# Kernel optimization log

Measured on AMD Instinct MI355X. Metric: run time of the kernel, lower is better.

The kernel has to match this reference:

```python
import jax, jax.numpy as jnp
from jax import lax
import numpy as np

DN = ('NCHW', 'OIHW', 'NCHW')

def conv(x, w, b, stride, pad):
    y = lax.conv_general_dilated(x, w, (stride, stride), [(pad, pad), (pad, pad)], dimension_numbers=DN)
    return y + b[None, :, None, None]

def conv_t(x, w, b, stride, pad):
    # PyTorch ConvTranspose2d weight layout is (in, out, kh, kw); flip spatially, swap to OIHW,
    # and realize transpose-conv as lhs-dilated conv with padding k-1-p.
    k = w.shape[2]
    wt = jnp.flip(w, (2, 3)).transpose(1, 0, 2, 3)
    q = k - 1 - pad
    y = lax.conv_general_dilated(x, wt, (1, 1), [(q, q), (q, q)], lhs_dilation=(stride, stride), dimension_numbers=DN)
    return y + b[None, :, None, None]

def setup_inputs() -> dict:
    key = jax.random.key(0)
    ks = jax.random.split(key, 16)
    K, C = 512, 64
    def he(k, shape, fan_in):
        return jax.random.normal(k, shape, jnp.float32) * np.float32(np.sqrt(2.0 / fan_in))
    return {
        'x': jax.random.normal(ks[0], (64, 1, 256, 256), jnp.float32),
        'e1_w': he(ks[1], (32, 1, 4, 4), 1 * 16), 'e1_b': jnp.zeros((32,), jnp.float32),
        'e2_w': he(ks[2], (64, 32, 4, 4), 32 * 16), 'e2_b': jnp.zeros((64,), jnp.float32),
        'e3_w': he(ks[3], (64, 64, 3, 3), 64 * 9), 'e3_b': jnp.zeros((64,), jnp.float32),
        'emb': jax.random.uniform(ks[4], (K, C), jnp.float32, -1.0 / K, 1.0 / K),
        'd1_w': he(ks[5], (64, 32, 3, 3), 64 * 9), 'd1_b': jnp.zeros((32,), jnp.float32),
        'd2_w': he(ks[6], (32, 64, 4, 4), 32 * 16), 'd2_b': jnp.zeros((64,), jnp.float32),
        'd3_w': he(ks[7], (64, 1, 4, 4), 64 * 16), 'd3_b': jnp.zeros((1,), jnp.float32),
    }

def reference(x, e1_w, e1_b, e2_w, e2_b, e3_w, e3_b, emb, d1_w, d1_b, d2_w, d2_b, d3_w, d3_b):
    # encoder
    h = jax.nn.relu(conv(x, e1_w, e1_b, 2, 1))
    h = jax.nn.relu(conv(h, e2_w, e2_b, 2, 1))
    ze = jax.nn.relu(conv(h, e3_w, e3_b, 1, 1))  # (N, C, H, W)
    N, C, H, W = ze.shape
    # VQ: nearest codebook entry per spatial location via ||z||^2 - 2 z.e + ||e||^2
    zf = ze.transpose(0, 2, 3, 1).reshape(-1, C)  # (N*H*W, C)
    dist = (zf * zf).sum(-1, keepdims=True) - 2.0 * (zf @ emb.T) + (emb * emb).sum(-1)[None, :]
    idx = jnp.argmin(dist, axis=1)  # (N*H*W,)
    zq = emb[idx].reshape(N, H, W, C).transpose(0, 3, 1, 2)  # (N, C, H, W)
    # straight-through estimator
    dec_in = ze + lax.stop_gradient(zq - ze)
    # decoder
    h = jax.nn.relu(conv_t(dec_in, d1_w, d1_b, 1, 1))
    h = jax.nn.relu(conv_t(h, d2_w, d2_b, 2, 1))
    x_hat = conv_t(h, d3_w, d3_b, 2, 1)
    return (x_hat, ze, zq)
```

## Files before the change

kernel.cpp:

```cpp
#include <hip/hip_runtime.h>

typedef short short8 __attribute__((ext_vector_type(8)));
typedef float f32x4 __attribute__((ext_vector_type(4)));

union U8 { short8 s8; unsigned int u[4]; };

__device__ __forceinline__ unsigned short f2bf(float f) {
    unsigned int u = __float_as_uint(f);
    u = (u + 0x7fffu + ((u >> 16) & 1u)) >> 16;
    return (unsigned short)u;
}
__device__ __forceinline__ float bf2f(unsigned short s) {
    return __uint_as_float(((unsigned int)s) << 16);
}


__global__ __launch_bounds__(256) void k_e1i(
    const float* __restrict__ x, const float* __restrict__ e1w, const float* __restrict__ e1b,
    unsigned short* __restrict__ h1p2, unsigned int* __restrict__ ws_dw,
    const float* __restrict__ e2w, const float* __restrict__ e3w,
    const float* __restrict__ d1w, const float* __restrict__ d2w,
    const float* __restrict__ d3w, const float* __restrict__ emb,
    unsigned short* __restrict__ ape2, unsigned short* __restrict__ ape3,
    unsigned short* __restrict__ apd1, unsigned short* __restrict__ apd2,
    unsigned short* __restrict__ apd3, unsigned short* __restrict__ embbf,
    float* __restrict__ hninit)
{
    int bid = blockIdx.x;
    if (bid < 4096) {
        int idx = bid * 256 + threadIdx.x;
        int ow = idx & 127, oh = (idx >> 7) & 127, n = idx >> 14;
        const float* xn = x + (size_t)n * 65536;
        float patch[16];
#pragma unroll
        for (int kh = 0; kh < 4; kh++) {
            int ih = 2 * oh + kh - 1;
#pragma unroll
            for (int kw = 0; kw < 4; kw++) {
                int iw = 2 * ow + kw - 1;
                bool ok = ((unsigned)ih < 256u) & ((unsigned)iw < 256u);
                patch[kh * 4 + kw] = ok ? xn[ih * 256 + iw] : 0.f;
            }
        }
        unsigned int outw[16];
#pragma unroll
        for (int oc = 0; oc < 32; oc++) {
            float acc = e1b[oc];
#pragma unroll
            for (int t = 0; t < 16; t++) acc += patch[t] * e1w[oc * 16 + t];
            unsigned short bf = f2bf(fmaxf(acc, 0.f));
            if (oc & 1) outw[oc >> 1] |= ((unsigned int)bf) << 16;
            else        outw[oc >> 1] = bf;
        }
        int par = ow & 1;
        int cidx = (ow + par) >> 1;
        size_t base = ((size_t)((idx >> 14) * 130 + oh + 1) * 2 + par) * 2112 + cidx * 32;
        uint4* dst = (uint4*)(h1p2 + base);
#pragma unroll
        for (int i = 0; i < 4; i++) dst[i] = *(uint4*)&outw[i * 4];
        return;
    }
    if (bid < 11376) {
        int t = (bid - 4096) * 256 + threadIdx.x;
        if (t < 270336) {
            int img = t / 4224, q = t % 4224;
            int rowsel = q / 2112, rem = q % 2112;
            ws_dw[img * 274560 + rowsel * 129 * 2112 + rem] = 0u;
        } else if (t < 532480) {
            int g = t - 270336;
            int img = g / 4096, q = g % 4096;
            int row = 1 + (q >> 5), c2 = q & 31;
            int sel = c2 >> 4, ch = c2 & 15;
            int par = sel ? 0 : 1, idx2 = sel ? 64 : 0;
            ws_dw[img * 274560 + row * 2112 + par * 1056 + idx2 * 16 + ch] = 0u;
        } else if (t < 1863680) {
            unsigned int base, Cd, r;
            if (t < 1064960)      { base = 17571840u; Cd = 32; r = t - 532480;  }
            else if (t < 1597440) { base = 34881536u; Cd = 32; r = t - 1064960; }
            else                  { base = 43802624u; Cd = 16; r = t - 1597440; }
            unsigned int per_img = 260u * Cd;
            unsigned int img = r / per_img, q = r % per_img;
            unsigned int p = q / Cd, c = q % Cd;
            unsigned int row, col;
            if (p < 66u)        { row = 0;  col = p; }
            else if (p < 132u)  { row = 65; col = p - 66u; }
            else { unsigned int s = p - 132u; row = 1 + (s >> 1); col = (s & 1) ? 65u : 0u; }
            ws_dw[base + ((img * 66u + row) * 66u + col) * Cd + c] = 0u;
        }
        return;
    }
    int f = (bid - 11376) * 256 + threadIdx.x;
    if (f < 4096) {
        int ks = f >> 8, mt = (f >> 6) & 3, lane = f & 63;
        int quad = lane >> 4, l16 = lane & 15;
        int oc = mt * 16 + l16, kh = ks >> 2, kw = ks & 3;
        short8 sv;
#pragma unroll
        for (int j = 0; j < 8; j++) {
            int ic = quad * 8 + j;
            sv[j] = (short)f2bf(e2w[((oc * 32 + ic) * 4 + kh) * 4 + kw]);
        }
        ((short8*)ape2)[f] = sv;
    } else if (f < 8704) {
        int g = f - 4096;
        int ks = g >> 8, mt = (g >> 6) & 3, lane = g & 63;
        int quad = lane >> 4, l16 = lane & 15;
        int oc = mt * 16 + l16, tap = ks >> 1, kh = tap / 3, kw = tap % 3;
        int icb = (ks & 1) * 32 + quad * 8;
        short8 sv;
#pragma unroll
        for (int j = 0; j < 8; j++)
            sv[j] = (short)f2bf(e3w[((oc * 64 + icb + j) * 3 + kh) * 3 + kw]);
        ((short8*)ape3)[g] = sv;
    } else if (f < 11008) {
        int g = f - 8704;
        int ks = g >> 7, mt = (g >> 6) & 1, lane = g & 63;
        int quad = lane >> 4, l16 = lane & 15;
        int oc = mt * 16 + l16, tap = ks >> 1, kh = tap / 3, kw = tap % 3;
        int icb = (ks & 1) * 32 + quad * 8;
        short8 sv;
#pragma unroll
        for (int j = 0; j < 8; j++)
            sv[j] = (short)f2bf(d1w[(((icb + j) * 32 + oc) * 3 + (2 - kh)) * 3 + (2 - kw)]);
        ((short8*)apd1)[g] = sv;
    } else if (f < 15104) {
        int g = f - 11008;
        int par = g >> 10, ks = (g >> 8) & 3, mt = (g >> 6) & 3, lane = g & 63;
        int quad = lane >> 4, l16 = lane & 15;
        int ph = par >> 1, pw = par & 1, a = ks >> 1, bb = ks & 1;
        int kh = 3 - ph - 2 * a, kw = 3 - pw - 2 * bb;
        int oc = mt * 16 + l16;
        short8 sv;
#pragma unroll
        for (int j = 0; j < 8; j++) {
            int ic = quad * 8 + j;
            sv[j] = (short)f2bf(d2w[((ic * 64 + oc) * 4 + kh) * 4 + kw]);
        }
        ((short8*)apd2)[g] = sv;
    } else if (f < 15232) {
        int g = f - 15104;
        int ks = g >> 6, lane = g & 63;
        int quad = lane >> 4, tap = lane & 15;
        short8 sv;
#pragma unroll
        for (int j = 0; j < 8; j++) {
            int ic = ks * 32 + quad * 8 + j;
            sv[j] = (short)f2bf(d3w[ic * 16 + tap]);
        }
        ((short8*)apd3)[g] = sv;
    } else if (f < 19328) {
        int g = f - 15232;
        int code = g >> 3, chb = (g & 7) * 8;
        short8 sv;
#pragma unroll
        for (int j = 0; j < 8; j++) sv[j] = (short)f2bf(emb[code * 64 + chb + j]);
        ((short8*)embbf)[g] = sv;
    } else if (f < 19840) {
        int code = f - 19328;
        float s = 0.f;
        for (int c = 0; c < 64; c++) { float v = emb[code * 64 + c]; s += v * v; }
        hninit[code] = 2.0f - 0.5f * s;
    }
}

template<int CIN, int COUT, int KSTEPS, int NCH, int WPIN, int MODE>
__global__ __launch_bounds__(256, 4) void k_conv(const unsigned short* __restrict__ inp,
                                                 const unsigned short* __restrict__ aprep,
                                                 const float* __restrict__ bias,
                                                 unsigned short* __restrict__ out0) {
    constexpr int MT = COUT / 16;
    constexpr int KCH = KSTEPS / NCH;
    __shared__ short8 sA[KCH * MT * 64];
    int tid = threadIdx.x;
    int wave = tid >> 6, lane = tid & 63, quad = lane >> 4, l16 = lane & 15;
    int bid = blockIdx.x;
    int n = bid >> 4, rg = bid & 15;
    int oh = rg * 4 + wave;

    int base0;
    if (MODE == 0) base0 = (n * 130 + 2 * oh) * 4224 + quad * 8;
    else           base0 = n * (WPIN * WPIN * CIN) + ((oh + 1) * WPIN + 1) * CIN + quad * 8;

    f32x4 acc[4][MT];
#pragma unroll
    for (int t = 0; t < 4; t++)
#pragma unroll
        for (int mt = 0; mt < MT; mt++)
            acc[t][mt] = *(const f32x4*)(bias + mt * 16 + quad * 4);

#pragma unroll
    for (int ch = 0; ch < NCH; ch++) {
        for (int i = tid; i < KCH * MT * 64; i += 256)
            sA[i] = ((const short8*)aprep)[ch * (KCH * MT * 64) + i];
        __syncthreads();
#pragma unroll
        for (int k = 0; k < KCH; k++) {
            int ks = ch * KCH + k;
            int off, pxs;
            if (MODE == 0) {
                int kh = ks >> 2, kw = ks & 3;
                int par = (kw & 1) ^ 1;
                off = kh * 4224 + par * 2112 + (kw >> 1) * 32;
                pxs = 32;
            } else {
                int tap = ks >> 1, kh = tap / 3, kw = tap % 3;
                off = ((kh - 1) * WPIN + (kw - 1)) * CIN + (ks & 1) * 32;
                pxs = CIN;
            }
            short8 bfr[4];
#pragma unroll
            for (int t = 0; t < 4; t++)
                bfr[t] = *(const short8*)(inp + base0 + (t * 16 + l16) * pxs + off);
#pragma unroll
            for (int mt = 0; mt < MT; mt++) {
                short8 a = sA[(k * MT + mt) * 64 + lane];
#pragma unroll
                for (int t = 0; t < 4; t++)
                    acc[t][mt] = __builtin_amdgcn_mfma_f32_16x16x32_bf16(a, bfr[t], acc[t][mt], 0, 0, 0);
            }
        }
        if (ch + 1 < NCH) __syncthreads();
    }

#pragma unroll
    for (int t = 0; t < 4; t++) {
        int ow = t * 16 + l16;
#pragma unroll
        for (int mt = 0; mt < MT; mt++) {
            float v0 = fmaxf(acc[t][mt][0], 0.f), v1 = fmaxf(acc[t][mt][1], 0.f);
            float v2 = fmaxf(acc[t][mt][2], 0.f), v3 = fmaxf(acc[t][mt][3], 0.f);
            unsigned int lo = (unsigned int)f2bf(v0) | ((unsigned int)f2bf(v1) << 16);
            unsigned int hi = (unsigned int)f2bf(v2) | ((unsigned int)f2bf(v3) << 16);
            uint2 uu; uu.x = lo; uu.y = hi;
            int oc = mt * 16 + quad * 4;
            if (MODE == 0) {
                size_t addr = (size_t)n * 278784 + ((oh + 1) * 66 + ow + 1) * 64 + oc;
                *(uint2*)(out0 + addr) = uu;
            } else {
                size_t addr = (size_t)n * 139392 + ((oh + 1) * 66 + ow + 1) * 32 + oc;
                *(uint2*)(out0 + addr) = uu;
            }
        }
    }
}

__global__ __launch_bounds__(256, 4) void k_e3vq(const unsigned short* __restrict__ h2p,
                                                 const unsigned short* __restrict__ ape3,
                                                 const float* __restrict__ bias,
                                                 const unsigned short* __restrict__ embbf,
                                                 const float* __restrict__ hninit,
                                                 float* __restrict__ ze_out,
                                                 float* __restrict__ zq_out,
                                                 unsigned short* __restrict__ zqp) {
    __shared__ __align__(16) char smem[36864];
    short8* sA = (short8*)smem;
    char*   sC = smem;

    int tid = threadIdx.x;
    int wave = tid >> 6, lane = tid & 63, quad = lane >> 4, l16 = lane & 15;
    int bid = blockIdx.x;
    int n = bid >> 4, rg = bid & 15;
    int oh = rg * 4 + wave;
    int base0 = n * 278784 + ((oh + 1) * 66 + 1) * 64 + quad * 8;

    f32x4 acc[4][4];
#pragma unroll
    for (int t = 0; t < 4; t++)
#pragma unroll
        for (int mt = 0; mt < 4; mt++)
            acc[t][mt] = *(const f32x4*)(bias + mt * 16 + quad * 4);

#pragma unroll
    for (int ch = 0; ch < 2; ch++) {
        for (int i = tid; i < 9 * 4 * 64; i += 256)
            sA[i] = ((const short8*)ape3)[ch * (9 * 4 * 64) + i];
        __syncthreads();
#pragma unroll
        for (int k = 0; k < 9; k++) {
            int ks = ch * 9 + k;
            int tap = ks >> 1, kh = tap / 3, kw = tap % 3;
            int off = ((kh - 1) * 66 + (kw - 1)) * 64 + (ks & 1) * 32;
            short8 bfr[4];
#pragma unroll
            for (int t = 0; t < 4; t++)
                bfr[t] = *(const short8*)(h2p + base0 + (t * 16 + l16) * 64 + off);
#pragma unroll
            for (int mt = 0; mt < 4; mt++) {
                short8 a = sA[(k * 4 + mt) * 64 + lane];
#pragma unroll
                for (int t = 0; t < 4; t++)
                    acc[t][mt] = __builtin_amdgcn_mfma_f32_16x16x32_bf16(a, bfr[t], acc[t][mt], 0, 0, 0);
            }
        }
        if (ch == 0) __syncthreads();
    }

#pragma unroll
    for (int t = 0; t < 4; t++)
#pragma unroll
        for (int mt = 0; mt < 4; mt++)
#pragma unroll
            for (int r = 0; r < 4; r++)
                acc[t][mt][r] = fmaxf(acc[t][mt][r], 0.f);

#pragma unroll
    for (int t = 0; t < 4; t++) {
        int px = oh * 64 + t * 16 + l16;
#pragma unroll
        for (int mt = 0; mt < 4; mt++) {
            int oc = mt * 16 + quad * 4;
#pragma unroll
            for (int r = 0; r < 4; r++)
                __builtin_nontemporal_store(acc[t][mt][r], &ze_out[((size_t)n * 64 + oc + r) * 4096 + px]);
        }
    }

    short8 b0[4], b1[4];
    int s0 = (((2 * quad) & 3) << 4) | l16;
    int s1 = (((2 * quad + 1) & 3) << 4) | l16;
#pragma unroll
    for (int t = 0; t < 4; t++) {
        f32x4 xv = (quad < 2) ? acc[t][0] : acc[t][1];
        f32x4 yv = (quad < 2) ? acc[t][2] : acc[t][3];
        unsigned int xa = (unsigned int)f2bf(xv[0]) | ((unsigned int)f2bf(xv[1]) << 16);
        unsigned int xb = (unsigned int)f2bf(xv[2]) | ((unsigned int)f2bf(xv[3]) << 16);
        unsigned int ya = (unsigned int)f2bf(yv[0]) | ((unsigned int)f2bf(yv[1]) << 16);
        unsigned int yb = (unsigned int)f2bf(yv[2]) | ((unsigned int)f2bf(yv[3]) << 16);
        U8 ub0, ub1;
        ub0.u[0] = (unsigned int)__shfl((int)xa, s0); ub0.u[1] = (unsigned int)__shfl((int)xb, s0);
        ub0.u[2] = (unsigned int)__shfl((int)xa, s1); ub0.u[3] = (unsigned int)__shfl((int)xb, s1);
        ub1.u[0] = (unsigned int)__shfl((int)ya, s0); ub1.u[1] = (unsigned int)__shfl((int)yb, s0);
        ub1.u[2] = (unsigned int)__shfl((int)ya, s1); ub1.u[3] = (unsigned int)__shfl((int)yb, s1);
        b0[t] = ub0.s8; b1[t] = ub1.s8;
    }

    unsigned int bk[4] = {0u, 0u, 0u, 0u};
#pragma unroll 1
    for (int cb = 0; cb < 4; cb++) {
        __syncthreads();
        {
            int r = tid >> 1, h = tid & 1;
            const uint4* src = (const uint4*)embbf;
#pragma unroll
            for (int i = 0; i < 4; i++) {
                uint4 v = src[cb * 1024 + tid * 4 + i];
                int slot = 4 * h + i;
                *(uint4*)(sC + r * 128 + ((slot ^ (r & 7)) << 4)) = v;
            }
        }
        __syncthreads();
#pragma unroll 2
        for (int jj = 0; jj < 8; jj++) {
            int j0 = cb * 128 + jj * 16;
            int rr = jj * 16 + l16;
            int sw = (rr & 7) << 4;
            short8 a0 = *(const short8*)(sC + rr * 128 + (((quad << 4)) ^ sw));
            short8 a1 = *(const short8*)(sC + rr * 128 + ((((quad + 4) << 4)) ^ sw));
            f32x4 ci = *(const f32x4*)(hninit + j0 + quad * 4);
            int iv = 511 - j0 - quad * 4;
#pragma unroll
            for (int t = 0; t < 4; t++) {
                f32x4 s = __builtin_amdgcn_mfma_f32_16x16x32_bf16(a0, b0[t], ci, 0, 0, 0);
                s = __builtin_amdgcn_mfma_f32_16x16x32_bf16(a1, b1[t], s, 0, 0, 0);
#pragma unroll
                for (int r = 0; r < 4; r++) {
                    unsigned int key = (__float_as_uint(s[r]) & 0xFFFFFE00u) | (unsigned int)(iv - r);
                    bk[t] = bk[t] > key ? bk[t] : key;
                }
            }
        }
    }
#pragma unroll
    for (int t = 0; t < 4; t++) {
        unsigned int o1 = (unsigned int)__shfl_xor((int)bk[t], 16);
        bk[t] = bk[t] > o1 ? bk[t] : o1;
        unsigned int o2 = (unsigned int)__shfl_xor((int)bk[t], 32);
        bk[t] = bk[t] > o2 ? bk[t] : o2;
    }
#pragma unroll
    for (int t = 0; t < 4; t++) {
        int code = 511 - (int)(bk[t] & 511u);
        int col = t * 16 + l16;
        int hw = oh * 64 + col;
        uint4 u0 = *(const uint4*)(embbf + code * 64 + quad * 16);
        uint4 u1 = *(const uint4*)(embbf + code * 64 + quad * 16 + 8);
        size_t qaddr = (size_t)n * 278784 + ((oh + 1) * 66 + (col + 1)) * 64 + quad * 16;
        *(uint4*)(zqp + qaddr) = u0;
        *(uint4*)(zqp + qaddr + 8) = u1;
        size_t zb = ((size_t)n * 64 + quad * 16) * 4096 + hw;
        unsigned int uw[8] = {u0.x, u0.y, u0.z, u0.w, u1.x, u1.y, u1.z, u1.w};
#pragma unroll
        for (int i = 0; i < 8; i++) {
            __builtin_nontemporal_store(__uint_as_float(uw[i] << 16), &zq_out[zb + (2 * i + 0) * 4096]);
            __builtin_nontemporal_store(__uint_as_float(uw[i] & 0xFFFF0000u), &zq_out[zb + (2 * i + 1) * 4096]);
        }
    }
}

__global__ __launch_bounds__(256, 4) void k_d2f(const unsigned short* __restrict__ d1op,
                                                const unsigned short* __restrict__ apd2,
                                                const float* __restrict__ bias,
                                                const unsigned short* __restrict__ apd3,
                                                unsigned short* __restrict__ sc16) {
    __shared__ short8 sA[1024];
    int tid = threadIdx.x;
    int wave = tid >> 6, lane = tid & 63, quad = lane >> 4, l16 = lane & 15;
    int bid = blockIdx.x;
    int n = bid >> 6, par = (bid >> 4) & 3, rg = bid & 15;
    int oh = rg * 4 + wave;
    int ph = par >> 1, pw = par & 1;

    short8 pa0 = ((const short8*)apd3)[lane];
    short8 pa1 = ((const short8*)apd3)[64 + lane];

    for (int i = tid; i < 1024; i += 256) sA[i] = ((const short8*)apd2)[par * 1024 + i];
    __syncthreads();

    int base0 = n * 139392 + ((oh + ph) * 66 + pw) * 32 + quad * 8;
    f32x4 acc[4][4];
#pragma unroll
    for (int t = 0; t < 4; t++)
#pragma unroll
        for (int mt = 0; mt < 4; mt++)
            acc[t][mt] = *(const f32x4*)(bias + mt * 16 + quad * 4);

#pragma unroll
    for (int k = 0; k < 4; k++) {
        int a_ = k >> 1, bb = k & 1;
        int off = (a_ * 66 + bb) * 32;
        short8 bfr[4];
#pragma unroll
        for (int t = 0; t < 4; t++)
            bfr[t] = *(const short8*)(d1op + base0 + (t * 16 + l16) * 32 + off);
#pragma unroll
        for (int mt = 0; mt < 4; mt++) {
            short8 a = sA[(k * 4 + mt) * 64 + lane];
#pragma unroll
            for (int t = 0; t < 4; t++)
                acc[t][mt] = __builtin_amdgcn_mfma_f32_16x16x32_bf16(a, bfr[t], acc[t][mt], 0, 0, 0);
        }
    }

    int s0 = (((2 * quad) & 3) << 4) | l16;
    int s1 = (((2 * quad + 1) & 3) << 4) | l16;
    int oh_out = 2 * oh + ph;
#pragma unroll
    for (int t = 0; t < 4; t++) {
#pragma unroll
        for (int mt = 0; mt < 4; mt++)
#pragma unroll
            for (int r = 0; r < 4; r++)
                acc[t][mt][r] = fmaxf(acc[t][mt][r], 0.f);
        f32x4 xv = (quad < 2) ? acc[t][0] : acc[t][1];
        f32x4 yv = (quad < 2) ? acc[t][2] : acc[t][3];
        unsigned int xa = (unsigned int)f2bf(xv[0]) | ((unsigned int)f2bf(xv[1]) << 16);
        unsigned int xb = (unsigned int)f2bf(xv[2]) | ((unsigned int)f2bf(xv[3]) << 16);
        unsigned int ya = (unsigned int)f2bf(yv[0]) | ((unsigned int)f2bf(yv[1]) << 16);
        unsigned int yb = (unsigned int)f2bf(yv[2]) | ((unsigned int)f2bf(yv[3]) << 16);
        U8 ub0, ub1;
        ub0.u[0] = (unsigned int)__shfl((int)xa, s0); ub0.u[1] = (unsigned int)__shfl((int)xb, s0);
        ub0.u[2] = (unsigned int)__shfl((int)xa, s1); ub0.u[3] = (unsigned int)__shfl((int)xb, s1);
        ub1.u[0] = (unsigned int)__shfl((int)ya, s0); ub1.u[1] = (unsigned int)__shfl((int)yb, s0);
        ub1.u[2] = (unsigned int)__shfl((int)ya, s1); ub1.u[3] = (unsigned int)__shfl((int)yb, s1);
        f32x4 sc = {0.f, 0.f, 0.f, 0.f};
        sc = __builtin_amdgcn_mfma_f32_16x16x32_bf16(pa0, ub0.s8, sc, 0, 0, 0);
        sc = __builtin_amdgcn_mfma_f32_16x16x32_bf16(pa1, ub1.s8, sc, 0, 0, 0);
        int ow_out = 2 * (t * 16 + l16) + pw;
        int pbaseo = n * 16384 + oh_out * 128 + ow_out;
#pragma unroll
        for (int r = 0; r < 4; r++) {
            int tap = quad * 4 + r;
            sc16[(size_t)tap * 1048576 + pbaseo] = f2bf(sc[r]);
        }
    }
}

__global__ __launch_bounds__(256) void k_d3e(const unsigned short* __restrict__ sc16,
                                             const float* __restrict__ d3b,
                                             float* __restrict__ xhat) {
    int idx = blockIdx.x * 256 + threadIdx.x;
    int ow = idx & 255, oh = (idx >> 8) & 255, n = idx >> 16;
    float acc = d3b[0];
    int kh0 = (oh + 1) & 1, kw0 = (ow + 1) & 1;
#pragma unroll
    for (int dh = 0; dh < 2; dh++) {
        int kh = kh0 + 2 * dh;
        int ih = (oh + 1 - kh) >> 1;
        bool vh = ((unsigned)ih < 128u);
#pragma unroll
        for (int dw = 0; dw < 2; dw++) {
            int kw = kw0 + 2 * dw;
            int iw = (ow + 1 - kw) >> 1;
            if (vh && ((unsigned)iw < 128u))
                acc += bf2f(sc16[(size_t)(kh * 4 + kw) * 1048576 + n * 16384 + ih * 128 + iw]);
        }
    }
    __builtin_nontemporal_store(acc, &xhat[(size_t)n * 65536 + oh * 256 + ow]);
}

extern "C" void kernel_launch(void* const* d_in, const int* in_sizes, int n_in,
                              void* d_out, int out_size, void* d_ws, size_t ws_size,
                              hipStream_t stream) {
    const float* x    = (const float*)d_in[0];
    const float* e1w  = (const float*)d_in[1];
    const float* e1b  = (const float*)d_in[2];
    const float* e2w  = (const float*)d_in[3];
    const float* e2b  = (const float*)d_in[4];
    const float* e3w  = (const float*)d_in[5];
    const float* e3b  = (const float*)d_in[6];
    const float* emb  = (const float*)d_in[7];
    const float* d1w  = (const float*)d_in[8];
    const float* d1b  = (const float*)d_in[9];
    const float* d2w  = (const float*)d_in[10];
    const float* d2b  = (const float*)d_in[11];
    const float* d3w  = (const float*)d_in[12];
    const float* d3b  = (const float*)d_in[13];

    float* xhat = (float*)d_out;
    float* ze   = xhat + 4194304;
    float* zq   = ze + 16777216;

    char* ws = (char*)d_ws;
    unsigned short* h1p2   = (unsigned short*)(ws + 0);
    unsigned short* h2p    = (unsigned short*)(ws + 70287360);
    unsigned short* zqp    = (unsigned short*)(ws + 139526144);
    unsigned short* d1op   = (unsigned short*)(ws + 175210496);
    unsigned short* sc16   = (unsigned short*)(ws + 193052672);
    unsigned short* ape2   = (unsigned short*)(ws + 226607104);
    unsigned short* ape3   = (unsigned short*)(ws + 226672640);
    unsigned short* apd1   = (unsigned short*)(ws + 226746368);
    unsigned short* apd2   = (unsigned short*)(ws + 226783232);
    unsigned short* apd3   = (unsigned short*)(ws + 226848768);
    unsigned short* embbf  = (unsigned short*)(ws + 226850816);
    float*          hninit = (float*)(ws + 226916352);

    k_e1i<<<11454, 256, 0, stream>>>(x, e1w, e1b, h1p2, (unsigned int*)d_ws,
                                     e2w, e3w, d1w, d2w, d3w, emb,
                                     ape2, ape3, apd1, apd2, apd3, embbf, hninit);
    k_conv<32, 64, 16, 2, 0, 0><<<1024, 256, 0, stream>>>(h1p2, ape2, e2b, h2p);
    k_e3vq<<<1024, 256, 0, stream>>>(h2p, ape3, e3b, embbf, hninit, ze, zq, zqp);
    k_conv<64, 32, 18, 2, 66, 2><<<1024, 256, 0, stream>>>(zqp, apd1, d1b, d1op);
    k_d2f<<<4096, 256, 0, stream>>>(d1op, apd2, d2b, apd3, sc16);
    k_d3e<<<16384, 256, 0, stream>>>(sc16, d3b, xhat);
}
```

Before: 402.3 us.

## Split fused e3 conv + VQ kernel into separate conv and VQ kernels

The fused e3-conv/VQ kernel is split in two. The first computes the e3 conv, writes ze, and stores the bf16 MFMA B-operand fragments to a scratch buffer that reuses the h1 workspace. A second kernel with twice as many blocks and higher occupancy (launch bounds 8) loads those fragments and runs the codebook argmin with half the tiles per wave. This aims to raise parallelism and occupancy in the VQ search, at the cost of an extra launch, a global round trip for the fragments, and reloading the codebook into LDS across more blocks.

```diff
diff --git a/kernel.cpp b/kernel.cpp
--- a/kernel.cpp
+++ b/kernel.cpp
@@ -244,18 +244,12 @@
     }
 }
 
-__global__ __launch_bounds__(256, 4) void k_e3vq(const unsigned short* __restrict__ h2p,
-                                                 const unsigned short* __restrict__ ape3,
-                                                 const float* __restrict__ bias,
-                                                 const unsigned short* __restrict__ embbf,
-                                                 const float* __restrict__ hninit,
-                                                 float* __restrict__ ze_out,
-                                                 float* __restrict__ zq_out,
-                                                 unsigned short* __restrict__ zqp) {
-    __shared__ __align__(16) char smem[36864];
-    short8* sA = (short8*)smem;
-    char*   sC = smem;
-
+__global__ __launch_bounds__(256, 4) void k_e3c(const unsigned short* __restrict__ h2p,
+                                                const unsigned short* __restrict__ ape3,
+                                                const float* __restrict__ bias,
+                                                float* __restrict__ ze_out,
+                                                unsigned short* __restrict__ bmat) {
+    __shared__ short8 sA[9 * 4 * 64];
     int tid = threadIdx.x;
     int wave = tid >> 6, lane = tid & 63, quad = lane >> 4, l16 = lane & 15;
     int bid = blockIdx.x;
@@ -315,9 +309,10 @@
         }
     }
 
-    short8 b0[4], b1[4];
     int s0 = (((2 * quad) & 3) << 4) | l16;
     int s1 = (((2 * quad + 1) & 3) << 4) | l16;
+    short8* bm = (short8*)bmat;
+    int wid = bid * 4 + wave;
 #pragma unroll
     for (int t = 0; t < 4; t++) {
         f32x4 xv = (quad < 2) ? acc[t][0] : acc[t][1];
@@ -331,10 +326,33 @@
         ub0.u[2] = (unsigned int)__shfl((int)xa, s1); ub0.u[3] = (unsigned int)__shfl((int)xb, s1);
         ub1.u[0] = (unsigned int)__shfl((int)ya, s0); ub1.u[1] = (unsigned int)__shfl((int)yb, s0);
         ub1.u[2] = (unsigned int)__shfl((int)ya, s1); ub1.u[3] = (unsigned int)__shfl((int)yb, s1);
-        b0[t] = ub0.s8; b1[t] = ub1.s8;
-    }
-
-    unsigned int bk[4] = {0u, 0u, 0u, 0u};
+        bm[((size_t)wid * 8 + 2 * t) * 64 + lane] = ub0.s8;
+        bm[((size_t)wid * 8 + 2 * t + 1) * 64 + lane] = ub1.s8;
+    }
+}
+
+__global__ __launch_bounds__(256, 8) void k_vq(const unsigned short* __restrict__ bmat,
+                                               const unsigned short* __restrict__ embbf,
+                                               const float* __restrict__ hninit,
+                                               float* __restrict__ zq_out,
+                                               unsigned short* __restrict__ zqp) {
+    __shared__ __align__(16) char sC[16384];
+    int tid = threadIdx.x;
+    int wave = tid >> 6, lane = tid & 63, quad = lane >> 4, l16 = lane & 15;
+    int bid = blockIdx.x;
+    int ow = bid * 2 + (wave >> 1);
+    int tp = wave & 1;
+
+    const short8* bm = (const short8*)bmat;
+    short8 b0[2], b1[2];
+#pragma unroll
+    for (int tt = 0; tt < 2; tt++) {
+        int t = tp * 2 + tt;
+        b0[tt] = bm[((size_t)ow * 8 + 2 * t) * 64 + lane];
+        b1[tt] = bm[((size_t)ow * 8 + 2 * t + 1) * 64 + lane];
+    }
+
+    unsigned int bk[2] = {0u, 0u};
 #pragma unroll 1
     for (int cb = 0; cb < 4; cb++) {
         __syncthreads();
@@ -354,32 +372,36 @@
             int j0 = cb * 128 + jj * 16;
             int rr = jj * 16 + l16;
             int sw = (rr & 7) << 4;
-            short8 a0 = *(const short8*)(sC + rr * 128 + (((quad << 4)) ^ sw));
-            short8 a1 = *(const short8*)(sC + rr * 128 + ((((quad + 4) << 4)) ^ sw));
+            short8 a0 = *(const short8*)(sC + rr * 128 + ((quad << 4) ^ sw));
+            short8 a1 = *(const short8*)(sC + rr * 128 + (((quad + 4) << 4) ^ sw));
             f32x4 ci = *(const f32x4*)(hninit + j0 + quad * 4);
             int iv = 511 - j0 - quad * 4;
 #pragma unroll
-            for (int t = 0; t < 4; t++) {
-                f32x4 s = __builtin_amdgcn_mfma_f32_16x16x32_bf16(a0, b0[t], ci, 0, 0, 0);
-                s = __builtin_amdgcn_mfma_f32_16x16x32_bf16(a1, b1[t], s, 0, 0, 0);
+            for (int tt = 0; tt < 2; tt++) {
+                f32x4 s = __builtin_amdgcn_mfma_f32_16x16x32_bf16(a0, b0[tt], ci, 0, 0, 0);
+                s = __builtin_amdgcn_mfma_f32_16x16x32_bf16(a1, b1[tt], s, 0, 0, 0);
 #pragma unroll
                 for (int r = 0; r < 4; r++) {
                     unsigned int key = (__float_as_uint(s[r]) & 0xFFFFFE00u) | (unsigned int)(iv - r);
-                    bk[t] = bk[t] > key ? bk[t] : key;
+                    bk[tt] = bk[tt] > key ? bk[tt] : key;
                 }
             }
         }
     }
 #pragma unroll
-    for (int t = 0; t < 4; t++) {
-        unsigned int o1 = (unsigned int)__shfl_xor((int)bk[t], 16);
-        bk[t] = bk[t] > o1 ? bk[t] : o1;
-        unsigned int o2 = (unsigned int)__shfl_xor((int)bk[t], 32);
-        bk[t] = bk[t] > o2 ? bk[t] : o2;
-    }
-#pragma unroll
-    for (int t = 0; t < 4; t++) {
-        int code = 511 - (int)(bk[t] & 511u);
+    for (int tt = 0; tt < 2; tt++) {
+        unsigned int o1 = (unsigned int)__shfl_xor((int)bk[tt], 16);
+        bk[tt] = bk[tt] > o1 ? bk[tt] : o1;
+        unsigned int o2 = (unsigned int)__shfl_xor((int)bk[tt], 32);
+        bk[tt] = bk[tt] > o2 ? bk[tt] : o2;
+    }
+
+    int n = ow >> 6, rg = (ow >> 2) & 15;
+    int oh = rg * 4 + (ow & 3);
+#pragma unroll
+    for (int tt = 0; tt < 2; tt++) {
+        int t = tp * 2 + tt;
+        int code = 511 - (int)(bk[tt] & 511u);
         int col = t * 16 + l16;
         int hw = oh * 64 + col;
         uint4 u0 = *(const uint4*)(embbf + code * 64 + quad * 16);
@@ -533,12 +555,14 @@
     unsigned short* apd3   = (unsigned short*)(ws + 226848768);
     unsigned short* embbf  = (unsigned short*)(ws + 226850816);
     float*          hninit = (float*)(ws + 226916352);
+    unsigned short* bmat   = h1p2;
 
     k_e1i<<<11454, 256, 0, stream>>>(x, e1w, e1b, h1p2, (unsigned int*)d_ws,
                                      e2w, e3w, d1w, d2w, d3w, emb,
                                      ape2, ape3, apd1, apd2, apd3, embbf, hninit);
     k_conv<32, 64, 16, 2, 0, 0><<<1024, 256, 0, stream>>>(h1p2, ape2, e2b, h2p);
-    k_e3vq<<<1024, 256, 0, stream>>>(h2p, ape3, e3b, embbf, hninit, ze, zq, zqp);
+    k_e3c<<<1024, 256, 0, stream>>>(h2p, ape3, e3b, ze, bmat);
+    k_vq<<<2048, 256, 0, stream>>>(bmat, embbf, hninit, zq, zqp);
     k_conv<64, 32, 18, 2, 66, 2><<<1024, 256, 0, stream>>>(zqp, apd1, d1b, d1op);
     k_d2f<<<4096, 256, 0, stream>>>(d1op, apd2, d2b, apd3, sc16);
     k_d3e<<<16384, 256, 0, stream>>>(sc16, d3b, xhat);
```

Result: slower. 419.2 us (+4.2%).
